# Kernel optimization log

Hardware: AMD Instinct MI355X
Metric: run time of the kernel (lower is better)

Reference implementation:

```python
import jax, jax.numpy as jnp
import numpy as np

T, B, E, H, R, NHASH, CHUNK = 2048, 2, 1024, 8, 2, 8, 32
D = E // H
INF = 1.0e16  # module's self.inf
BIG = 1.0e8   # module's self.big


def setup_inputs() -> dict:
    key = jax.random.key(0)
    ks = jax.random.split(key, 8)
    w = lambda k, shape, s=0.02: jax.random.normal(k, shape, dtype=jnp.float32) * s
    return {
        "query": jax.random.normal(ks[0], (T, B, E), jnp.float32),
        "key":   jax.random.normal(ks[1], (T, B, E), jnp.float32),
        "value": jax.random.normal(ks[2], (T, B, E), jnp.float32),
        "Wq": w(ks[3], (E, E)), "bq": jnp.zeros((E,), jnp.float32),
        "Wv": w(ks[4], (E, E)), "bv": jnp.zeros((E,), jnp.float32),
        "Wo": w(ks[5], (E, E)), "bo": jnp.zeros((E,), jnp.float32),
        "hash_w": w(ks[6], (R, H, D, NHASH // 2), 0.1),
    }


def _hashes(x_tbhd, hash_w):
    # einsum('ibnf,rnfh->ibrnh'), cat([lin,-lin]), argmax -> [T,B,R,H]
    lin = jnp.einsum('tbhd,rhdn->tbrhn', x_tbhd, hash_w)
    return jnp.argmax(jnp.concatenate([lin, -lin], axis=-1), axis=-1)


def _gather_t(x_bhtd, perm_brht):
    # gather along T with per-(b,r,h) permutation -> [B,R,H,T,D]
    Bb, Rr, Hh, Tt = perm_brht.shape
    Dd = x_bhtd.shape[-1]
    xb = jnp.broadcast_to(x_bhtd[:, None], (Bb, Rr, Hh, Tt, Dd))
    idx = jnp.broadcast_to(perm_brht[..., None], (Bb, Rr, Hh, Tt, Dd))
    return jnp.take_along_axis(xb, idx, axis=3)


def reference(query, key, value, Wq, bq, Wv, bv, Wo, bo, hash_w):
    del key  # share_kq=True (self-attention): keys are L2-normalized queries
    scaling = D ** -0.5
    qf = query @ Wq + bq                                    # [T,B,E]
    kf = qf / jnp.linalg.norm(qf, axis=-1, keepdims=True)   # F.normalize over embed dim
    vf = value @ Wv + bv
    q = qf.reshape(T, B, H, D) * scaling
    k = kf.reshape(T, B, H, D)
    v = vf.reshape(T, B, H, D)

    q_hash = _hashes(q, hash_w)                             # [T,B,R,H]
    k_hash = _hashes(k, hash_w)

    qh_t = jnp.transpose(q_hash, (1, 2, 3, 0))              # [B,R,H,T]
    kh_t = jnp.transpose(k_hash, (1, 2, 3, 0))
    p_q = jnp.argsort(qh_t, axis=-1)                        # stable sort by hash
    p_k = jnp.argsort(kh_t, axis=-1)
    inv_q = jnp.argsort(p_q, axis=-1)                       # sorted position of each token

    q_s = _gather_t(jnp.transpose(q, (1, 2, 0, 3)), p_q)    # [B,R,H,T,D]
    k_s = _gather_t(jnp.transpose(k, (1, 2, 0, 3)), p_k)
    v_s = _gather_t(jnp.transpose(v, (1, 2, 0, 3)), p_k)
    qh_s = jnp.take_along_axis(qh_t, p_q, axis=-1)
    kh_s = jnp.take_along_axis(kh_t, p_k, axis=-1)

    C = T // CHUNK
    M = 3 * CHUNK
    chunk = lambda x: x.reshape(x.shape[:3] + (C, CHUNK) + x.shape[4:])
    q_c, qh_c, qid_c = chunk(q_s), chunk(qh_s), chunk(p_q)
    k_c, v_c, kh_c, kid_c = chunk(k_s), chunk(v_s), chunk(kh_s), chunk(p_k)

    # each query chunk attends key chunks {c-1, c, c+1} (num_chunk_offsets=3, wraparound)
    blocks = lambda x: jnp.concatenate([jnp.roll(x, 1, axis=3), x, jnp.roll(x, -1, axis=3)], axis=4)
    kb, vb, khb, kidb = blocks(k_c), blocks(v_c), blocks(kh_c), blocks(kid_c)

    scores = jnp.einsum('brhcld,brhcmd->brhclm', q_c, kb)   # q pre-scaled by d^-0.5
    scores = scores - INF * (qh_c[..., :, None] != khb[..., None, :])   # mask_different_hashes
    scores = scores - BIG * (qid_c[..., :, None] == kidb[..., None, :]) # mask_current

    # cross-round duplicate counting: key ids attended per original query
    chunk_of = inv_q // CHUNK                               # [B,R,H,T]
    idx = jnp.broadcast_to(chunk_of[..., None], (B, R, H, T, M))
    A = jnp.take_along_axis(kidb, idx, axis=3)              # [B,R,H,T,M]
    dup = []
    for r in range(R):
        c = jnp.zeros((B, H, T, M), jnp.int32)
        for r2 in range(R):
            c = c + (A[:, r, :, :, :, None] == A[:, r2, :, :, None, :]).sum(-1, dtype=jnp.int32)
        dup.append(c)
    dup = jnp.stack(dup, axis=1)                            # [B,R,H,T,M]
    idx2 = jnp.broadcast_to(p_q[..., None], (B, R, H, T, M))
    dup_s = jnp.take_along_axis(dup, idx2, axis=3)          # sorted-query order
    scores = scores - jnp.log(dup_s.astype(scores.dtype)).reshape(scores.shape)

    z = jax.nn.logsumexp(scores, axis=-1)                   # [B,R,H,C,L]
    attn = jax.nn.softmax(scores, axis=-1)
    o = jnp.einsum('brhclm,brhcmd->brhcld', attn, vb).reshape(B, R, H, T, D)
    z = z.reshape(B, R, H, T)

    # scatter back to original token order
    idx3 = jnp.broadcast_to(inv_q[..., None], (B, R, H, T, D))
    o = jnp.take_along_axis(o, idx3, axis=3)
    z = jnp.take_along_axis(z, inv_q, axis=3)

    w = jax.nn.softmax(z, axis=1)                           # combine rounds by logsumexp weight
    out = (w[..., None] * o).sum(axis=1)                    # [B,H,T,D]
    out = jnp.transpose(out, (2, 0, 1, 3)).reshape(T, B, E)
    return out @ Wo + bo
```

## Files before the change

kernel.cpp:

```cpp
#include <hip/hip_runtime.h>

typedef unsigned short ushort_t;
typedef __bf16 bf16x8 __attribute__((ext_vector_type(8)));
typedef float f32x4 __attribute__((ext_vector_type(4)));

#define T_DIM 2048
#define B_DIM 2
#define E_DIM 1024
#define H_DIM 8
#define R_DIM 2
#define D_DIM 128
#define M_WIN 96
#define SCALING 0.08838834764831845f
#define LN2F 0.69314718055994530942f

__device__ __forceinline__ float bfu(unsigned u) {
  union { unsigned i; float f; } x; x.i = u << 16; return x.f;
}
__device__ __forceinline__ unsigned f2bf(float f) {
  union { float f; unsigned i; } x; x.f = f;
  unsigned r = x.i + 0x7fffu + ((x.i >> 16) & 1u);
  return r >> 16;
}
__device__ __forceinline__ void gl_lds16(const void* g, void* l) {
  __builtin_amdgcn_global_load_lds(
      (const __attribute__((address_space(1))) unsigned int*)g,
      (__attribute__((address_space(3))) unsigned int*)l, 16, 0, 0);
}

__global__ __launch_bounds__(256) void pack2_kernel(const float* __restrict__ in,
                                                    ushort_t* __restrict__ hi,
                                                    ushort_t* __restrict__ lo)
{
  int i = (blockIdx.x * 256 + threadIdx.x) * 4;
  float4 v = *(const float4*)&in[i];
  unsigned h0 = f2bf(v.x), h1 = f2bf(v.y), h2 = f2bf(v.z), h3 = f2bf(v.w);
  uint2 oh; oh.x = h0 | (h1 << 16); oh.y = h2 | (h3 << 16);
  *(uint2*)&hi[i] = oh;
  unsigned l0 = f2bf(v.x - bfu(h0)), l1 = f2bf(v.y - bfu(h1));
  unsigned l2 = f2bf(v.z - bfu(h2)), l3 = f2bf(v.w - bfu(h3));
  uint2 ol; ol.x = l0 | (l1 << 16); ol.y = l2 | (l3 << 16);
  *(uint2*)&lo[i] = ol;
}

__global__ __launch_bounds__(256) void pack1_kernel(const float* __restrict__ in,
                                                    ushort_t* __restrict__ hi)
{
  int i = (blockIdx.x * 256 + threadIdx.x) * 4;
  float4 v = *(const float4*)&in[i];
  uint2 oh;
  oh.x = f2bf(v.x) | (f2bf(v.y) << 16);
  oh.y = f2bf(v.z) | (f2bf(v.w) << 16);
  *(uint2*)&hi[i] = oh;
}

__global__ __launch_bounds__(256) void packT_kernel(const float* __restrict__ in,
                                                    ushort_t* __restrict__ hi,
                                                    ushort_t* __restrict__ lo,
                                                    int Kk, int Nn)
{
  __shared__ float tile[64][65];
  const int tid = threadIdx.x;
  const int k0 = blockIdx.y * 64, n0 = blockIdx.x * 64;
  const int tr = tid >> 4, tc4 = (tid & 15) * 4;
#pragma unroll
  for (int rr = 0; rr < 64; rr += 16)
    *(float4*)&tile[tr + rr][tc4] = *(const float4*)&in[(size_t)(k0 + tr + rr) * Nn + n0 + tc4];
  __syncthreads();
#pragma unroll
  for (int rr = 0; rr < 64; rr += 16) {
    int n = n0 + tr + rr;
    float v0 = tile[tc4 + 0][tr + rr];
    float v1 = tile[tc4 + 1][tr + rr];
    float v2 = tile[tc4 + 2][tr + rr];
    float v3 = tile[tc4 + 3][tr + rr];
    unsigned h0 = f2bf(v0), h1 = f2bf(v1), h2 = f2bf(v2), h3 = f2bf(v3);
    uint2 oh; oh.x = h0 | (h1 << 16); oh.y = h2 | (h3 << 16);
    *(uint2*)&hi[(size_t)n * Kk + k0 + tc4] = oh;
    if (lo) {
      uint2 ol;
      ol.x = f2bf(v0 - bfu(h0)) | (f2bf(v1 - bfu(h1)) << 16);
      ol.y = f2bf(v2 - bfu(h2)) | (f2bf(v3 - bfu(h3)) << 16);
      *(uint2*)&lo[(size_t)n * Kk + k0 + tc4] = ol;
    }
  }
}

__global__ __launch_bounds__(256) void gemm_mfma(
    const ushort_t* __restrict__ Ah, const ushort_t* __restrict__ Al,
    const ushort_t* __restrict__ Bh, const ushort_t* __restrict__ Bl,
    const float* __restrict__ bias, float* __restrict__ C,
    int Mm, int Nn, int Kk)
{
  __shared__ ushort_t As[128 * 32];
  __shared__ ushort_t Bs[64 * 32];
  __shared__ ushort_t As2[128 * 32];
  __shared__ ushort_t Bs2[64 * 32];
  const int tid = threadIdx.x;
  const int w = tid >> 6, lane = tid & 63;
  const int lm = lane & 15, quad = lane >> 4;
  const int wr = w >> 1, wc = w & 1;
  const int m0 = blockIdx.y * 128, n0 = blockIdx.x * 64;
  const bool three = (Al != nullptr);

  f32x4 acc[4][2] = {};

  for (int k0 = 0; k0 < Kk; k0 += 32) {
    __syncthreads();
#pragma unroll
    for (int j = 0; j < 2; ++j) {
      int g = j * 256 + w * 64 + lane;
      gl_lds16(Ah + (size_t)(m0 + (g >> 2)) * Kk + k0 + (g & 3) * 8,
               &As[(size_t)(j * 256 + w * 64) * 8]);
    }
    {
      int g = w * 64 + lane;
      gl_lds16(Bh + (size_t)(n0 + (g >> 2)) * Kk + k0 + (g & 3) * 8,
               &Bs[(size_t)(w * 64) * 8]);
    }
    if (three) {
#pragma unroll
      for (int j = 0; j < 2; ++j) {
        int g = j * 256 + w * 64 + lane;
        gl_lds16(Al + (size_t)(m0 + (g >> 2)) * Kk + k0 + (g & 3) * 8,
                 &As2[(size_t)(j * 256 + w * 64) * 8]);
      }
      int g = w * 64 + lane;
      gl_lds16(Bl + (size_t)(n0 + (g >> 2)) * Kk + k0 + (g & 3) * 8,
               &Bs2[(size_t)(w * 64) * 8]);
    }
    __syncthreads();

    bf16x8 av[4], bv[2];
#pragma unroll
    for (int i = 0; i < 4; ++i) av[i] = *(const bf16x8*)&As[(wr * 64 + i * 16 + lm) * 32 + quad * 8];
#pragma unroll
    for (int j = 0; j < 2; ++j) bv[j] = *(const bf16x8*)&Bs[(wc * 32 + j * 16 + lm) * 32 + quad * 8];
    if (three) {
      bf16x8 av2[4], bv2[2];
#pragma unroll
      for (int i = 0; i < 4; ++i) av2[i] = *(const bf16x8*)&As2[(wr * 64 + i * 16 + lm) * 32 + quad * 8];
#pragma unroll
      for (int j = 0; j < 2; ++j) bv2[j] = *(const bf16x8*)&Bs2[(wc * 32 + j * 16 + lm) * 32 + quad * 8];
#pragma unroll
      for (int i = 0; i < 4; ++i)
#pragma unroll
        for (int j = 0; j < 2; ++j) {
          acc[i][j] = __builtin_amdgcn_mfma_f32_16x16x32_bf16(av[i], bv[j], acc[i][j], 0, 0, 0);
          acc[i][j] = __builtin_amdgcn_mfma_f32_16x16x32_bf16(av2[i], bv[j], acc[i][j], 0, 0, 0);
          acc[i][j] = __builtin_amdgcn_mfma_f32_16x16x32_bf16(av[i], bv2[j], acc[i][j], 0, 0, 0);
        }
    } else {
#pragma unroll
      for (int i = 0; i < 4; ++i)
#pragma unroll
        for (int j = 0; j < 2; ++j)
          acc[i][j] = __builtin_amdgcn_mfma_f32_16x16x32_bf16(av[i], bv[j], acc[i][j], 0, 0, 0);
    }
  }

#pragma unroll
  for (int j = 0; j < 2; ++j) {
    int col = n0 + wc * 32 + j * 16 + lm;
    float bj = bias[col];
#pragma unroll
    for (int i = 0; i < 4; ++i)
#pragma unroll
      for (int rg = 0; rg < 4; ++rg)
        C[(size_t)(m0 + wr * 64 + i * 16 + quad * 4 + rg) * Nn + col] = acc[i][j][rg] + bj;
  }
}

__global__ __launch_bounds__(256) void norm_kernel(const float* __restrict__ qf,
                                                   float* __restrict__ inv_nrm)
{
  int row = blockIdx.x, tid = threadIdx.x;
  const float* r = qf + (size_t)row * E_DIM;
  float4 v = *(const float4*)(r + tid * 4);
  float s = v.x * v.x + v.y * v.y + v.z * v.z + v.w * v.w;
  for (int off = 1; off < 64; off <<= 1) s += __shfl_xor(s, off);
  __shared__ float part[4];
  if ((tid & 63) == 0) part[tid >> 6] = s;
  __syncthreads();
  if (tid == 0) {
    float t = part[0] + part[1] + part[2] + part[3];
    inv_nrm[row] = 1.0f / sqrtf(t);
  }
}

__global__ __launch_bounds__(256) void hash_kernel(const float* __restrict__ qf,
                                                   const float* __restrict__ hw,
                                                   int* __restrict__ hashb)
{
  __shared__ float wlds[16 * 516];
  const int tid = threadIdx.x;
  for (int i = tid; i < 8192; i += 256) wlds[(i >> 9) * 516 + (i & 511)] = hw[i];
  __syncthreads();
  const int rloc = tid >> 4, rh = tid & 15;
  const int r = rh >> 3, h = rh & 7;
  const int row = blockIdx.x * 16 + rloc;
  const float* qrow = qf + (size_t)row * E_DIM + h * D_DIM;
  const float* wp = &wlds[rh * 516];
  float a0 = 0.f, a1 = 0.f, a2 = 0.f, a3 = 0.f;
  for (int d = 0; d < 128; d += 4) {
    float4 q4 = *(const float4*)&qrow[d];
    float4 w0 = *(const float4*)&wp[d * 4];
    float4 w1 = *(const float4*)&wp[d * 4 + 4];
    float4 w2 = *(const float4*)&wp[d * 4 + 8];
    float4 w3 = *(const float4*)&wp[d * 4 + 12];
    a0 += q4.x * w0.x + q4.y * w1.x + q4.z * w2.x + q4.w * w3.x;
    a1 += q4.x * w0.y + q4.y * w1.y + q4.z * w2.y + q4.w * w3.y;
    a2 += q4.x * w0.z + q4.y * w1.z + q4.z * w2.z + q4.w * w3.z;
    a3 += q4.x * w0.w + q4.y * w1.w + q4.z * w2.w + q4.w * w3.w;
  }
  float lin[4] = {a0, a1, a2, a3};
  float best = lin[0]; int bi = 0;
#pragma unroll
  for (int idx = 1; idx < 8; ++idx) {
    float v = (idx < 4) ? lin[idx] : -lin[idx - 4];
    if (v > best) { best = v; bi = idx; }
  }
  int t = row >> 1, b = row & 1;
  hashb[(size_t)((b * R_DIM + r) * H_DIM + h) * T_DIM + t] = bi;
}

__global__ __launch_bounds__(256) void sort_kernel(const int* __restrict__ hashb,
                                                   int* __restrict__ p, int* __restrict__ inv)
{
  const int bid = blockIdx.x, tid = threadIdx.x;
  const int lane = tid & 63, w = tid >> 6;
  const int* hrow = hashb + (size_t)bid * T_DIM;
  __shared__ int mat[8][256];
  __shared__ int btot[8], bbase[8];
  int cnt[8];
#pragma unroll
  for (int v = 0; v < 8; ++v) cnt[v] = 0;
  int hv[8];
#pragma unroll
  for (int j = 0; j < 8; ++j) { hv[j] = hrow[tid * 8 + j]; cnt[hv[j]]++; }
#pragma unroll
  for (int v = 0; v < 8; ++v) mat[v][tid] = cnt[v];
  __syncthreads();
  for (int v = w; v < 8; v += 4) {
    int4 c4 = *(const int4*)&mat[v][lane * 4];
    int s = c4.x + c4.y + c4.z + c4.w;
    int x = s;
    for (int off = 1; off < 64; off <<= 1) {
      int y = __shfl_up(x, off);
      if (lane >= off) x += y;
    }
    int excl = x - s;
    mat[v][lane * 4 + 0] = excl;
    mat[v][lane * 4 + 1] = excl + c4.x;
    mat[v][lane * 4 + 2] = excl + c4.x + c4.y;
    mat[v][lane * 4 + 3] = excl + c4.x + c4.y + c4.z;
    if (lane == 63) btot[v] = x;
  }
  __syncthreads();
  if (tid == 0) {
    int run = 0;
    for (int v = 0; v < 8; ++v) { bbase[v] = run; run += btot[v]; }
  }
  __syncthreads();
#pragma unroll
  for (int v = 0; v < 8; ++v) cnt[v] = 0;
#pragma unroll
  for (int j = 0; j < 8; ++j) {
    int v = hv[j];
    int pos = bbase[v] + mat[v][tid] + cnt[v];
    cnt[v]++;
    p[(size_t)bid * T_DIM + pos] = tid * 8 + j;
    inv[(size_t)bid * T_DIM + tid * 8 + j] = pos;
  }
}

__global__ __launch_bounds__(256) void attn_kernel(
    const float* __restrict__ qf, const float* __restrict__ vf,
    const float* __restrict__ inv_nrm, const int* __restrict__ hashb,
    const int* __restrict__ p, const int* __restrict__ inv,
    float* __restrict__ o_out, float* __restrict__ z_out)
{
  const int c = blockIdx.x, h = blockIdx.y, bz = blockIdx.z;
  const int b = bz >> 1, r = bz & 1;
  const int brh = (b * R_DIM + r) * H_DIM + h;
  const int brh_o = (b * R_DIM + (r ^ 1)) * H_DIM + h;
  const int tid = threadIdx.x;
  const int lane = tid & 63, w = tid >> 6;
  const int lm = lane & 15, quad = lane >> 4;

  __shared__ __align__(16) unsigned char smem[45824];
  ushort_t* Qs = (ushort_t*)smem;
  ushort_t* Ks = (ushort_t*)(smem + 8704);
  ushort_t* VT = (ushort_t*)smem;
  float*    SS = (float*)(smem + 26624);
  ushort_t* Ps = (ushort_t*)(smem + 39168);
  __shared__ int sq_id[32], sq_h[32], cq_o[32];
  __shared__ int sk_id[M_WIN], sk_h[M_WIN], ck_o[M_WIN];
  __shared__ float s_invn[M_WIN];

  if (tid < M_WIN) {
    int m = tid;
    int chunk = (c + (m >> 5) + 63) & 63;
    int pos = chunk * 32 + (m & 31);
    int t = p[(size_t)brh * T_DIM + pos];
    sk_id[m] = t;
    sk_h[m] = hashb[(size_t)brh * T_DIM + t];
    ck_o[m] = inv[(size_t)brh_o * T_DIM + t] >> 5;
    s_invn[m] = inv_nrm[t * B_DIM + b];
    if (m < 32) {
      int tq = p[(size_t)brh * T_DIM + c * 32 + m];
      sq_id[m] = tq;
      sq_h[m] = hashb[(size_t)brh * T_DIM + tq];
      cq_o[m] = inv[(size_t)brh_o * T_DIM + tq] >> 5;
    }
  }
  __syncthreads();

  for (int idx = tid; idx < 1024; idx += 256) {
    int row = idx >> 5, seg = idx & 31;
    int t = sq_id[row];
    float4 v = *(const float4*)(qf + ((size_t)(t * B_DIM + b) << 10) + h * D_DIM + seg * 4);
    uint2 o2;
    o2.x = f2bf(v.x * SCALING) | (f2bf(v.y * SCALING) << 16);
    o2.y = f2bf(v.z * SCALING) | (f2bf(v.w * SCALING) << 16);
    *(uint2*)&Qs[row * 136 + seg * 4] = o2;
  }
  for (int idx = tid; idx < 3072; idx += 256) {
    int m = idx >> 5, seg = idx & 31;
    int t = sk_id[m];
    float inrm = s_invn[m];
    float4 v = *(const float4*)(qf + ((size_t)(t * B_DIM + b) << 10) + h * D_DIM + seg * 4);
    uint2 o2;
    o2.x = f2bf(v.x * inrm) | (f2bf(v.y * inrm) << 16);
    o2.y = f2bf(v.z * inrm) | (f2bf(v.w * inrm) << 16);
    *(uint2*)&Ks[m * 136 + seg * 4] = o2;
  }
  __syncthreads();

  const int mw = w & 1, nset = w >> 1;
  bf16x8 av[4];
#pragma unroll
  for (int kk = 0; kk < 4; ++kk)
    av[kk] = *(const bf16x8*)&Qs[(mw * 16 + lm) * 136 + kk * 32 + quad * 8];
  f32x4 sacc[3] = {};
#pragma unroll
  for (int jj = 0; jj < 3; ++jj) {
    int nt = nset * 3 + jj;
#pragma unroll
    for (int kk = 0; kk < 4; ++kk) {
      bf16x8 bv = *(const bf16x8*)&Ks[(nt * 16 + lm) * 136 + kk * 32 + quad * 8];
      sacc[jj] = __builtin_amdgcn_mfma_f32_16x16x32_bf16(av[kk], bv, sacc[jj], 0, 0, 0);
    }
  }
  __syncthreads();

  const int rowb = mw * 16 + quad * 4;
#pragma unroll
  for (int jj = 0; jj < 3; ++jj) {
    int col = (nset * 3 + jj) * 16 + lm;
    int kh = sk_h[col], kid = sk_id[col], kco = ck_o[col];
#pragma unroll
    for (int rg = 0; rg < 4; ++rg) {
      int row = rowb + rg;
      float sc = sacc[jj][rg];
      if (kh != sq_h[row]) sc -= 1.0e16f;
      if (kid == sq_id[row]) sc -= 1.0e8f;
      int dc = (kco - cq_o[row]) & 63;
      if (dc <= 1 || dc == 63) sc -= LN2F;
      SS[row * 98 + col] = sc;
    }
  }
  for (int idx = tid; idx < 3072; idx += 256) {
    int d = idx & 127, mg = idx >> 7;
    unsigned vv0, vv1, vv2, vv3;
    {
      int t0 = sk_id[mg * 4 + 0], t1 = sk_id[mg * 4 + 1];
      int t2 = sk_id[mg * 4 + 2], t3 = sk_id[mg * 4 + 3];
      const size_t off = (size_t)h * D_DIM + d;
      vv0 = f2bf(vf[((size_t)(t0 * B_DIM + b) << 10) + off]);
      vv1 = f2bf(vf[((size_t)(t1 * B_DIM + b) << 10) + off]);
      vv2 = f2bf(vf[((size_t)(t2 * B_DIM + b) << 10) + off]);
      vv3 = f2bf(vf[((size_t)(t3 * B_DIM + b) << 10) + off]);
    }
    uint2 o2; o2.x = vv0 | (vv1 << 16); o2.y = vv2 | (vv3 << 16);
    *(uint2*)&VT[d * 104 + mg * 4] = o2;
  }
  __syncthreads();

  {
    const int l = tid >> 3, g = tid & 7;
    float smy[12];
#pragma unroll
    for (int j = 0; j < 12; ++j) smy[j] = SS[l * 98 + g + 8 * j];
    float mx = smy[0];
#pragma unroll
    for (int j = 1; j < 12; ++j) mx = fmaxf(mx, smy[j]);
    mx = fmaxf(mx, __shfl_xor(mx, 1));
    mx = fmaxf(mx, __shfl_xor(mx, 2));
    mx = fmaxf(mx, __shfl_xor(mx, 4));
    float sum = 0.f, ey[12];
#pragma unroll
    for (int j = 0; j < 12; ++j) { ey[j] = expf(smy[j] - mx); sum += ey[j]; }
    sum += __shfl_xor(sum, 1);
    sum += __shfl_xor(sum, 2);
    sum += __shfl_xor(sum, 4);
    float inv_s = 1.0f / sum;
#pragma unroll
    for (int j = 0; j < 12; ++j)
      Ps[l * 104 + g + 8 * j] = (ushort_t)f2bf(ey[j] * inv_s);
    if (g == 0) z_out[(size_t)brh * T_DIM + sq_id[l]] = mx + logf(sum);
  }
  __syncthreads();

  const int dset = w >> 1;
  bf16x8 pa[3];
#pragma unroll
  for (int kk = 0; kk < 3; ++kk)
    pa[kk] = *(const bf16x8*)&Ps[(mw * 16 + lm) * 104 + kk * 32 + quad * 8];
  f32x4 oacc[4] = {};
#pragma unroll
  for (int jj = 0; jj < 4; ++jj) {
    int dt = dset * 4 + jj;
#pragma unroll
    for (int kk = 0; kk < 3; ++kk) {
      bf16x8 bv = *(const bf16x8*)&VT[(dt * 16 + lm) * 104 + kk * 32 + quad * 8];
      oacc[jj] = __builtin_amdgcn_mfma_f32_16x16x32_bf16(pa[kk], bv, oacc[jj], 0, 0, 0);
    }
  }
#pragma unroll
  for (int jj = 0; jj < 4; ++jj) {
    int col = (dset * 4 + jj) * 16 + lm;
#pragma unroll
    for (int rg = 0; rg < 4; ++rg) {
      int row = rowb + rg;
      int tqo = sq_id[row];
      o_out[((size_t)brh * T_DIM + tqo) * D_DIM + col] = oacc[jj][rg];
    }
  }
}

__global__ __launch_bounds__(256) void combine_kernel(const float* __restrict__ o_buf,
                                                      const float* __restrict__ z_buf,
                                                      ushort_t* __restrict__ ctx)
{
  int gid = blockIdx.x * 256 + threadIdx.x;
  int d = gid & 127;
  int t = (gid >> 7) & (T_DIM - 1);
  int h = (gid >> 18) & 7;
  int b = gid >> 21;
  int brh0 = (b * R_DIM + 0) * H_DIM + h;
  int brh1 = brh0 + H_DIM;
  float z0 = z_buf[(size_t)brh0 * T_DIM + t], z1 = z_buf[(size_t)brh1 * T_DIM + t];
  float mz = fmaxf(z0, z1);
  float e0 = expf(z0 - mz), e1 = expf(z1 - mz);
  float o0 = o_buf[((size_t)brh0 * T_DIM + t) * D_DIM + d];
  float o1 = o_buf[((size_t)brh1 * T_DIM + t) * D_DIM + d];
  float val = (e0 * o0 + e1 * o1) / (e0 + e1);
  ctx[((size_t)t * B_DIM + b) * E_DIM + h * D_DIM + d] = (ushort_t)f2bf(val);
}

extern "C" void kernel_launch(void* const* d_in, const int* in_sizes, int n_in,
                              void* d_out, int out_size, void* d_ws, size_t ws_size,
                              hipStream_t stream)
{
  const float* query = (const float*)d_in[0];
  const float* value = (const float*)d_in[2];
  const float* Wq = (const float*)d_in[3];
  const float* bq = (const float*)d_in[4];
  const float* Wv = (const float*)d_in[5];
  const float* bv = (const float*)d_in[6];
  const float* Wo = (const float*)d_in[7];
  const float* bo = (const float*)d_in[8];
  const float* hw = (const float*)d_in[9];

  float* ws = (float*)d_ws;
  float* qf      = ws;
  float* vf      = qf + 4194304;
  float* obuf    = vf + 4194304;
  float* zbuf    = obuf + 8388608;
  float* inv_nrm = zbuf + 65536;
  int*   hashb   = (int*)(inv_nrm + 4096);
  int*   pperm   = hashb + 65536;
  int*   pinv    = pperm + 65536;
  ushort_t* WqTh = (ushort_t*)(pinv + 65536);
  ushort_t* WqTl = WqTh + 1048576;
  ushort_t* WvTh = WqTl + 1048576;
  ushort_t* WoTh = WvTh + 1048576;
  ushort_t* qh  = (ushort_t*)obuf;
  ushort_t* ql  = qh + 4194304;
  ushort_t* vh  = ql + 4194304;
  ushort_t* ctx = (ushort_t*)qf;

  pack2_kernel<<<4096, 256, 0, stream>>>(query, qh, ql);
  pack1_kernel<<<4096, 256, 0, stream>>>(value, vh);
  packT_kernel<<<dim3(16, 16), 256, 0, stream>>>(Wq, WqTh, WqTl, 1024, 1024);
  packT_kernel<<<dim3(16, 16), 256, 0, stream>>>(Wv, WvTh, (ushort_t*)nullptr, 1024, 1024);
  packT_kernel<<<dim3(16, 16), 256, 0, stream>>>(Wo, WoTh, (ushort_t*)nullptr, 1024, 1024);
  gemm_mfma<<<dim3(16, 32), 256, 0, stream>>>(qh, ql, WqTh, WqTl, bq, qf, 4096, 1024, 1024);
  gemm_mfma<<<dim3(16, 32), 256, 0, stream>>>(vh, (ushort_t*)nullptr, WvTh, (ushort_t*)nullptr, bv, vf, 4096, 1024, 1024);
  norm_kernel<<<4096, 256, 0, stream>>>(qf, inv_nrm);
  hash_kernel<<<256, 256, 0, stream>>>(qf, hw, hashb);
  sort_kernel<<<32, 256, 0, stream>>>(hashb, pperm, pinv);
  attn_kernel<<<dim3(64, 8, 4), 256, 0, stream>>>(qf, vf, inv_nrm, hashb, pperm, pinv, obuf, zbuf);
  combine_kernel<<<16384, 256, 0, stream>>>(obuf, zbuf, ctx);
  gemm_mfma<<<dim3(16, 32), 256, 0, stream>>>(ctx, (ushort_t*)nullptr, WoTh, (ushort_t*)nullptr, bo, (float*)d_out, 4096, 1024, 1024);
}
```

Baseline: 283.1 us.

## Compute hashes from fused Wq·hash_w in fp32, drop split-bf16 Q GEMM, batch launches

Hash logits are now computed directly from the fp32 query times a precomputed Wq·hash_w matrix (plus bias term), so the Q projection GEMM no longer needs the three-pass hi/lo bf16 split for hash accuracy and runs as a plain bf16 GEMM. The Q and V GEMMs are merged into one launch via blockIdx.z, as are the pack kernels and the three weight transposes. The attention output buffer is stored in bf16, and combine is vectorized to four elements per thread. Key metadata is packed into one int per token to shrink shared memory. The cost is lower precision for Q/K in attention and for the per-round outputs, plus an extra small fp32 GEMM for hashing.

```diff
diff --git a/kernel.cpp b/kernel.cpp
--- a/kernel.cpp
+++ b/kernel.cpp
@@ -28,107 +28,163 @@
       (__attribute__((address_space(3))) unsigned int*)l, 16, 0, 0);
 }
 
-__global__ __launch_bounds__(256) void pack2_kernel(const float* __restrict__ in,
-                                                    ushort_t* __restrict__ hi,
-                                                    ushort_t* __restrict__ lo)
-{
-  int i = (blockIdx.x * 256 + threadIdx.x) * 4;
-  float4 v = *(const float4*)&in[i];
-  unsigned h0 = f2bf(v.x), h1 = f2bf(v.y), h2 = f2bf(v.z), h3 = f2bf(v.w);
-  uint2 oh; oh.x = h0 | (h1 << 16); oh.y = h2 | (h3 << 16);
-  *(uint2*)&hi[i] = oh;
-  unsigned l0 = f2bf(v.x - bfu(h0)), l1 = f2bf(v.y - bfu(h1));
-  unsigned l2 = f2bf(v.z - bfu(h2)), l3 = f2bf(v.w - bfu(h3));
-  uint2 ol; ol.x = l0 | (l1 << 16); ol.y = l2 | (l3 << 16);
-  *(uint2*)&lo[i] = ol;
-}
-
-__global__ __launch_bounds__(256) void pack1_kernel(const float* __restrict__ in,
-                                                    ushort_t* __restrict__ hi)
-{
-  int i = (blockIdx.x * 256 + threadIdx.x) * 4;
-  float4 v = *(const float4*)&in[i];
+__global__ __launch_bounds__(256) void packA_kernel(const float* __restrict__ q,
+                                                    const float* __restrict__ v,
+                                                    ushort_t* __restrict__ qh,
+                                                    ushort_t* __restrict__ vh)
+{
+  int bid = blockIdx.x;
+  const float* src = (bid < 4096) ? q : v;
+  ushort_t* dst = (bid < 4096) ? qh : vh;
+  int i = ((bid & 4095) * 256 + threadIdx.x) * 4;
+  float4 x = *(const float4*)&src[i];
   uint2 oh;
-  oh.x = f2bf(v.x) | (f2bf(v.y) << 16);
-  oh.y = f2bf(v.z) | (f2bf(v.w) << 16);
-  *(uint2*)&hi[i] = oh;
-}
-
-__global__ __launch_bounds__(256) void packT_kernel(const float* __restrict__ in,
-                                                    ushort_t* __restrict__ hi,
-                                                    ushort_t* __restrict__ lo,
-                                                    int Kk, int Nn)
-{
+  oh.x = f2bf(x.x) | (f2bf(x.y) << 16);
+  oh.y = f2bf(x.z) | (f2bf(x.w) << 16);
+  *(uint2*)&dst[i] = oh;
+}
+
+__global__ __launch_bounds__(256) void packT_kernel(
+    const float* __restrict__ w0, const float* __restrict__ w1,
+    const float* __restrict__ w2, ushort_t* __restrict__ o0,
+    ushort_t* __restrict__ o1, ushort_t* __restrict__ o2)
+{
+  const float* in = (blockIdx.z == 0) ? w0 : (blockIdx.z == 1) ? w1 : w2;
+  ushort_t* hi = (blockIdx.z == 0) ? o0 : (blockIdx.z == 1) ? o1 : o2;
   __shared__ float tile[64][65];
   const int tid = threadIdx.x;
   const int k0 = blockIdx.y * 64, n0 = blockIdx.x * 64;
   const int tr = tid >> 4, tc4 = (tid & 15) * 4;
 #pragma unroll
   for (int rr = 0; rr < 64; rr += 16)
-    *(float4*)&tile[tr + rr][tc4] = *(const float4*)&in[(size_t)(k0 + tr + rr) * Nn + n0 + tc4];
+    *(float4*)&tile[tr + rr][tc4] = *(const float4*)&in[(size_t)(k0 + tr + rr) * E_DIM + n0 + tc4];
   __syncthreads();
 #pragma unroll
   for (int rr = 0; rr < 64; rr += 16) {
     int n = n0 + tr + rr;
-    float v0 = tile[tc4 + 0][tr + rr];
-    float v1 = tile[tc4 + 1][tr + rr];
-    float v2 = tile[tc4 + 2][tr + rr];
-    float v3 = tile[tc4 + 3][tr + rr];
-    unsigned h0 = f2bf(v0), h1 = f2bf(v1), h2 = f2bf(v2), h3 = f2bf(v3);
-    uint2 oh; oh.x = h0 | (h1 << 16); oh.y = h2 | (h3 << 16);
-    *(uint2*)&hi[(size_t)n * Kk + k0 + tc4] = oh;
-    if (lo) {
-      uint2 ol;
-      ol.x = f2bf(v0 - bfu(h0)) | (f2bf(v1 - bfu(h1)) << 16);
-      ol.y = f2bf(v2 - bfu(h2)) | (f2bf(v3 - bfu(h3)) << 16);
-      *(uint2*)&lo[(size_t)n * Kk + k0 + tc4] = ol;
-    }
-  }
+    uint2 oh;
+    oh.x = f2bf(tile[tc4 + 0][tr + rr]) | (f2bf(tile[tc4 + 1][tr + rr]) << 16);
+    oh.y = f2bf(tile[tc4 + 2][tr + rr]) | (f2bf(tile[tc4 + 3][tr + rr]) << 16);
+    *(uint2*)&hi[(size_t)n * E_DIM + k0 + tc4] = oh;
+  }
+}
+
+__global__ __launch_bounds__(256) void fuseF_kernel(const float* __restrict__ Wq,
+                                                    const float* __restrict__ bq,
+                                                    const float* __restrict__ hw,
+                                                    float* __restrict__ F,
+                                                    float* __restrict__ cvec)
+{
+  __shared__ float wl[512];
+  const int rh = blockIdx.x, h = rh & 7;
+  const int tid = threadIdx.x;
+  for (int i = tid; i < 512; i += 256) wl[i] = hw[rh * 512 + i];
+  __syncthreads();
+  for (int e = tid; e < E_DIM; e += 256) {
+    const float* wr = Wq + (size_t)e * E_DIM + h * D_DIM;
+    float a0 = 0.f, a1 = 0.f, a2 = 0.f, a3 = 0.f;
+    for (int d = 0; d < 128; d += 4) {
+      float4 q4 = *(const float4*)&wr[d];
+      float4 w0 = *(const float4*)&wl[d * 4];
+      float4 w1 = *(const float4*)&wl[d * 4 + 4];
+      float4 w2 = *(const float4*)&wl[d * 4 + 8];
+      float4 w3 = *(const float4*)&wl[d * 4 + 12];
+      a0 += q4.x * w0.x + q4.y * w1.x + q4.z * w2.x + q4.w * w3.x;
+      a1 += q4.x * w0.y + q4.y * w1.y + q4.z * w2.y + q4.w * w3.y;
+      a2 += q4.x * w0.z + q4.y * w1.z + q4.z * w2.z + q4.w * w3.z;
+      a3 += q4.x * w0.w + q4.y * w1.w + q4.z * w2.w + q4.w * w3.w;
+    }
+    float4 o; o.x = a0; o.y = a1; o.z = a2; o.w = a3;
+    *(float4*)&F[(size_t)e * 64 + rh * 4] = o;
+  }
+  if (tid < 4) {
+    float acc = 0.f;
+    for (int d = 0; d < 128; ++d) acc += bq[h * D_DIM + d] * wl[d * 4 + tid];
+    cvec[rh * 4 + tid] = acc;
+  }
+}
+
+__global__ __launch_bounds__(256) void hashlin_kernel(const float* __restrict__ query,
+                                                      const float* __restrict__ F,
+                                                      const float* __restrict__ cvec,
+                                                      int* __restrict__ hashb)
+{
+  __shared__ float As[32][17];
+  __shared__ float Fs[32][64];
+  const int tid = threadIdx.x;
+  const int ty = tid >> 4, tx = tid & 15;
+  const int r0 = blockIdx.x * 16;
+  float acc0 = 0.f, acc1 = 0.f, acc2 = 0.f, acc3 = 0.f;
+  for (int k0 = 0; k0 < E_DIM; k0 += 32) {
+    __syncthreads();
+    {
+      int i = tid * 2, row = i >> 5, kk = i & 31;
+      float2 a2 = *(const float2*)&query[(size_t)(r0 + row) * E_DIM + k0 + kk];
+      As[kk][row] = a2.x; As[kk + 1][row] = a2.y;
+    }
+    {
+      int i = tid * 8, kk = i >> 6, cc = i & 63;
+      float4 f0 = *(const float4*)&F[(size_t)(k0 + kk) * 64 + cc];
+      float4 f1 = *(const float4*)&F[(size_t)(k0 + kk) * 64 + cc + 4];
+      *(float4*)&Fs[kk][cc] = f0;
+      *(float4*)&Fs[kk][cc + 4] = f1;
+    }
+    __syncthreads();
+#pragma unroll
+    for (int kk = 0; kk < 32; ++kk) {
+      float a = As[kk][ty];
+      float4 f4 = *(const float4*)&Fs[kk][tx * 4];
+      acc0 += a * f4.x; acc1 += a * f4.y; acc2 += a * f4.z; acc3 += a * f4.w;
+    }
+  }
+  float4 c4 = *(const float4*)&cvec[tx * 4];
+  float lin[4] = {acc0 + c4.x, acc1 + c4.y, acc2 + c4.z, acc3 + c4.w};
+  float best = lin[0]; int bi = 0;
+#pragma unroll
+  for (int idx = 1; idx < 8; ++idx) {
+    float v = (idx < 4) ? lin[idx] : -lin[idx - 4];
+    if (v > best) { best = v; bi = idx; }
+  }
+  int grow = r0 + ty;
+  int t = grow >> 1, b = grow & 1;
+  int rr = tx >> 3, hh = tx & 7;
+  hashb[(size_t)((b * R_DIM + rr) * H_DIM + hh) * T_DIM + t] = bi;
 }
 
 __global__ __launch_bounds__(256) void gemm_mfma(
-    const ushort_t* __restrict__ Ah, const ushort_t* __restrict__ Al,
-    const ushort_t* __restrict__ Bh, const ushort_t* __restrict__ Bl,
-    const float* __restrict__ bias, float* __restrict__ C,
-    int Mm, int Nn, int Kk)
-{
+    const ushort_t* __restrict__ A0, const ushort_t* __restrict__ B0,
+    const float* __restrict__ bias0, float* __restrict__ C0,
+    const ushort_t* __restrict__ A1, const ushort_t* __restrict__ B1,
+    const float* __restrict__ bias1, float* __restrict__ C1)
+{
+  const ushort_t* Ah = blockIdx.z ? A1 : A0;
+  const ushort_t* Bh = blockIdx.z ? B1 : B0;
+  const float* bias = blockIdx.z ? bias1 : bias0;
+  float* C = blockIdx.z ? C1 : C0;
+
   __shared__ ushort_t As[128 * 32];
   __shared__ ushort_t Bs[64 * 32];
-  __shared__ ushort_t As2[128 * 32];
-  __shared__ ushort_t Bs2[64 * 32];
   const int tid = threadIdx.x;
   const int w = tid >> 6, lane = tid & 63;
   const int lm = lane & 15, quad = lane >> 4;
   const int wr = w >> 1, wc = w & 1;
   const int m0 = blockIdx.y * 128, n0 = blockIdx.x * 64;
-  const bool three = (Al != nullptr);
 
   f32x4 acc[4][2] = {};
 
-  for (int k0 = 0; k0 < Kk; k0 += 32) {
+  for (int k0 = 0; k0 < E_DIM; k0 += 32) {
     __syncthreads();
 #pragma unroll
     for (int j = 0; j < 2; ++j) {
       int g = j * 256 + w * 64 + lane;
-      gl_lds16(Ah + (size_t)(m0 + (g >> 2)) * Kk + k0 + (g & 3) * 8,
+      gl_lds16(Ah + (size_t)(m0 + (g >> 2)) * E_DIM + k0 + (g & 3) * 8,
                &As[(size_t)(j * 256 + w * 64) * 8]);
     }
     {
       int g = w * 64 + lane;
-      gl_lds16(Bh + (size_t)(n0 + (g >> 2)) * Kk + k0 + (g & 3) * 8,
+      gl_lds16(Bh + (size_t)(n0 + (g >> 2)) * E_DIM + k0 + (g & 3) * 8,
                &Bs[(size_t)(w * 64) * 8]);
     }
-    if (three) {
-#pragma unroll
-      for (int j = 0; j < 2; ++j) {
-        int g = j * 256 + w * 64 + lane;
-        gl_lds16(Al + (size_t)(m0 + (g >> 2)) * Kk + k0 + (g & 3) * 8,
-                 &As2[(size_t)(j * 256 + w * 64) * 8]);
-      }
-      int g = w * 64 + lane;
-      gl_lds16(Bl + (size_t)(n0 + (g >> 2)) * Kk + k0 + (g & 3) * 8,
-               &Bs2[(size_t)(w * 64) * 8]);
-    }
     __syncthreads();
 
     bf16x8 av[4], bv[2];
@@ -136,27 +192,11 @@
     for (int i = 0; i < 4; ++i) av[i] = *(const bf16x8*)&As[(wr * 64 + i * 16 + lm) * 32 + quad * 8];
 #pragma unroll
     for (int j = 0; j < 2; ++j) bv[j] = *(const bf16x8*)&Bs[(wc * 32 + j * 16 + lm) * 32 + quad * 8];
-    if (three) {
-      bf16x8 av2[4], bv2[2];
-#pragma unroll
-      for (int i = 0; i < 4; ++i) av2[i] = *(const bf16x8*)&As2[(wr * 64 + i * 16 + lm) * 32 + quad * 8];
-#pragma unroll
-      for (int j = 0; j < 2; ++j) bv2[j] = *(const bf16x8*)&Bs2[(wc * 32 + j * 16 + lm) * 32 + quad * 8];
-#pragma unroll
-      for (int i = 0; i < 4; ++i)
-#pragma unroll
-        for (int j = 0; j < 2; ++j) {
-          acc[i][j] = __builtin_amdgcn_mfma_f32_16x16x32_bf16(av[i], bv[j], acc[i][j], 0, 0, 0);
-          acc[i][j] = __builtin_amdgcn_mfma_f32_16x16x32_bf16(av2[i], bv[j], acc[i][j], 0, 0, 0);
-          acc[i][j] = __builtin_amdgcn_mfma_f32_16x16x32_bf16(av[i], bv2[j], acc[i][j], 0, 0, 0);
-        }
-    } else {
-#pragma unroll
-      for (int i = 0; i < 4; ++i)
-#pragma unroll
-        for (int j = 0; j < 2; ++j)
-          acc[i][j] = __builtin_amdgcn_mfma_f32_16x16x32_bf16(av[i], bv[j], acc[i][j], 0, 0, 0);
-    }
+#pragma unroll
+    for (int i = 0; i < 4; ++i)
+#pragma unroll
+      for (int j = 0; j < 2; ++j)
+        acc[i][j] = __builtin_amdgcn_mfma_f32_16x16x32_bf16(av[i], bv[j], acc[i][j], 0, 0, 0);
   }
 
 #pragma unroll
@@ -167,7 +207,7 @@
     for (int i = 0; i < 4; ++i)
 #pragma unroll
       for (int rg = 0; rg < 4; ++rg)
-        C[(size_t)(m0 + wr * 64 + i * 16 + quad * 4 + rg) * Nn + col] = acc[i][j][rg] + bj;
+        C[(size_t)(m0 + wr * 64 + i * 16 + quad * 4 + rg) * E_DIM + col] = acc[i][j][rg] + bj;
   }
 }
 
@@ -188,42 +228,6 @@
   }
 }
 
-__global__ __launch_bounds__(256) void hash_kernel(const float* __restrict__ qf,
-                                                   const float* __restrict__ hw,
-                                                   int* __restrict__ hashb)
-{
-  __shared__ float wlds[16 * 516];
-  const int tid = threadIdx.x;
-  for (int i = tid; i < 8192; i += 256) wlds[(i >> 9) * 516 + (i & 511)] = hw[i];
-  __syncthreads();
-  const int rloc = tid >> 4, rh = tid & 15;
-  const int r = rh >> 3, h = rh & 7;
-  const int row = blockIdx.x * 16 + rloc;
-  const float* qrow = qf + (size_t)row * E_DIM + h * D_DIM;
-  const float* wp = &wlds[rh * 516];
-  float a0 = 0.f, a1 = 0.f, a2 = 0.f, a3 = 0.f;
-  for (int d = 0; d < 128; d += 4) {
-    float4 q4 = *(const float4*)&qrow[d];
-    float4 w0 = *(const float4*)&wp[d * 4];
-    float4 w1 = *(const float4*)&wp[d * 4 + 4];
-    float4 w2 = *(const float4*)&wp[d * 4 + 8];
-    float4 w3 = *(const float4*)&wp[d * 4 + 12];
-    a0 += q4.x * w0.x + q4.y * w1.x + q4.z * w2.x + q4.w * w3.x;
-    a1 += q4.x * w0.y + q4.y * w1.y + q4.z * w2.y + q4.w * w3.y;
-    a2 += q4.x * w0.z + q4.y * w1.z + q4.z * w2.z + q4.w * w3.z;
-    a3 += q4.x * w0.w + q4.y * w1.w + q4.z * w2.w + q4.w * w3.w;
-  }
-  float lin[4] = {a0, a1, a2, a3};
-  float best = lin[0]; int bi = 0;
-#pragma unroll
-  for (int idx = 1; idx < 8; ++idx) {
-    float v = (idx < 4) ? lin[idx] : -lin[idx - 4];
-    if (v > best) { best = v; bi = idx; }
-  }
-  int t = row >> 1, b = row & 1;
-  hashb[(size_t)((b * R_DIM + r) * H_DIM + h) * T_DIM + t] = bi;
-}
-
 __global__ __launch_bounds__(256) void sort_kernel(const int* __restrict__ hashb,
                                                    int* __restrict__ p, int* __restrict__ inv)
 {
@@ -278,7 +282,7 @@
     const float* __restrict__ qf, const float* __restrict__ vf,
     const float* __restrict__ inv_nrm, const int* __restrict__ hashb,
     const int* __restrict__ p, const int* __restrict__ inv,
-    float* __restrict__ o_out, float* __restrict__ z_out)
+    ushort_t* __restrict__ o_out, float* __restrict__ z_out)
 {
   const int c = blockIdx.x, h = blockIdx.y, bz = blockIdx.z;
   const int b = bz >> 1, r = bz & 1;
@@ -288,14 +292,13 @@
   const int lane = tid & 63, w = tid >> 6;
   const int lm = lane & 15, quad = lane >> 4;
 
-  __shared__ __align__(16) unsigned char smem[45824];
+  __shared__ __align__(16) unsigned char smem[39424];
   ushort_t* Qs = (ushort_t*)smem;
   ushort_t* Ks = (ushort_t*)(smem + 8704);
   ushort_t* VT = (ushort_t*)smem;
   float*    SS = (float*)(smem + 26624);
-  ushort_t* Ps = (ushort_t*)(smem + 39168);
-  __shared__ int sq_id[32], sq_h[32], cq_o[32];
-  __shared__ int sk_id[M_WIN], sk_h[M_WIN], ck_o[M_WIN];
+  ushort_t* Ps = (ushort_t*)(smem + 26624);
+  __shared__ int skp[M_WIN], sqp[32];
   __shared__ float s_invn[M_WIN];
 
   if (tid < M_WIN) {
@@ -303,22 +306,22 @@
     int chunk = (c + (m >> 5) + 63) & 63;
     int pos = chunk * 32 + (m & 31);
     int t = p[(size_t)brh * T_DIM + pos];
-    sk_id[m] = t;
-    sk_h[m] = hashb[(size_t)brh * T_DIM + t];
-    ck_o[m] = inv[(size_t)brh_o * T_DIM + t] >> 5;
+    int hh = hashb[(size_t)brh * T_DIM + t];
+    int co = inv[(size_t)brh_o * T_DIM + t] >> 5;
+    skp[m] = t | (hh << 11) | (co << 14);
     s_invn[m] = inv_nrm[t * B_DIM + b];
     if (m < 32) {
       int tq = p[(size_t)brh * T_DIM + c * 32 + m];
-      sq_id[m] = tq;
-      sq_h[m] = hashb[(size_t)brh * T_DIM + tq];
-      cq_o[m] = inv[(size_t)brh_o * T_DIM + tq] >> 5;
+      int qh = hashb[(size_t)brh * T_DIM + tq];
+      int qco = inv[(size_t)brh_o * T_DIM + tq] >> 5;
+      sqp[m] = tq | (qh << 11) | (qco << 14);
     }
   }
   __syncthreads();
 
   for (int idx = tid; idx < 1024; idx += 256) {
     int row = idx >> 5, seg = idx & 31;
-    int t = sq_id[row];
+    int t = sqp[row] & 2047;
     float4 v = *(const float4*)(qf + ((size_t)(t * B_DIM + b) << 10) + h * D_DIM + seg * 4);
     uint2 o2;
     o2.x = f2bf(v.x * SCALING) | (f2bf(v.y * SCALING) << 16);
@@ -327,7 +330,7 @@
   }
   for (int idx = tid; idx < 3072; idx += 256) {
     int m = idx >> 5, seg = idx & 31;
-    int t = sk_id[m];
+    int t = skp[m] & 2047;
     float inrm = s_invn[m];
     float4 v = *(const float4*)(qf + ((size_t)(t * B_DIM + b) << 10) + h * D_DIM + seg * 4);
     uint2 o2;
@@ -358,30 +361,27 @@
 #pragma unroll
   for (int jj = 0; jj < 3; ++jj) {
     int col = (nset * 3 + jj) * 16 + lm;
-    int kh = sk_h[col], kid = sk_id[col], kco = ck_o[col];
+    int kp = skp[col];
 #pragma unroll
     for (int rg = 0; rg < 4; ++rg) {
-      int row = rowb + rg;
+      int qp = sqp[rowb + rg];
       float sc = sacc[jj][rg];
-      if (kh != sq_h[row]) sc -= 1.0e16f;
-      if (kid == sq_id[row]) sc -= 1.0e8f;
-      int dc = (kco - cq_o[row]) & 63;
+      if ((kp ^ qp) & 0x3800) sc -= 1.0e16f;
+      if (!((kp ^ qp) & 0x7FF)) sc -= 1.0e8f;
+      int dc = ((kp >> 14) - (qp >> 14)) & 63;
       if (dc <= 1 || dc == 63) sc -= LN2F;
-      SS[row * 98 + col] = sc;
+      SS[(rowb + rg) * 100 + col] = sc;
     }
   }
   for (int idx = tid; idx < 3072; idx += 256) {
     int d = idx & 127, mg = idx >> 7;
-    unsigned vv0, vv1, vv2, vv3;
-    {
-      int t0 = sk_id[mg * 4 + 0], t1 = sk_id[mg * 4 + 1];
-      int t2 = sk_id[mg * 4 + 2], t3 = sk_id[mg * 4 + 3];
-      const size_t off = (size_t)h * D_DIM + d;
-      vv0 = f2bf(vf[((size_t)(t0 * B_DIM + b) << 10) + off]);
-      vv1 = f2bf(vf[((size_t)(t1 * B_DIM + b) << 10) + off]);
-      vv2 = f2bf(vf[((size_t)(t2 * B_DIM + b) << 10) + off]);
-      vv3 = f2bf(vf[((size_t)(t3 * B_DIM + b) << 10) + off]);
-    }
+    int t0 = skp[mg * 4 + 0] & 2047, t1 = skp[mg * 4 + 1] & 2047;
+    int t2 = skp[mg * 4 + 2] & 2047, t3 = skp[mg * 4 + 3] & 2047;
+    const size_t off = (size_t)h * D_DIM + d;
+    unsigned vv0 = f2bf(vf[((size_t)(t0 * B_DIM + b) << 10) + off]);
+    unsigned vv1 = f2bf(vf[((size_t)(t1 * B_DIM + b) << 10) + off]);
+    unsigned vv2 = f2bf(vf[((size_t)(t2 * B_DIM + b) << 10) + off]);
+    unsigned vv3 = f2bf(vf[((size_t)(t3 * B_DIM + b) << 10) + off]);
     uint2 o2; o2.x = vv0 | (vv1 << 16); o2.y = vv2 | (vv3 << 16);
     *(uint2*)&VT[d * 104 + mg * 4] = o2;
   }
@@ -391,7 +391,7 @@
     const int l = tid >> 3, g = tid & 7;
     float smy[12];
 #pragma unroll
-    for (int j = 0; j < 12; ++j) smy[j] = SS[l * 98 + g + 8 * j];
+    for (int j = 0; j < 12; ++j) smy[j] = SS[l * 100 + g + 8 * j];
     float mx = smy[0];
 #pragma unroll
     for (int j = 1; j < 12; ++j) mx = fmaxf(mx, smy[j]);
@@ -407,8 +407,8 @@
     float inv_s = 1.0f / sum;
 #pragma unroll
     for (int j = 0; j < 12; ++j)
-      Ps[l * 104 + g + 8 * j] = (ushort_t)f2bf(ey[j] * inv_s);
-    if (g == 0) z_out[(size_t)brh * T_DIM + sq_id[l]] = mx + logf(sum);
+      Ps[l * 200 + g + 8 * j] = (ushort_t)f2bf(ey[j] * inv_s);
+    if (g == 0) z_out[(size_t)brh * T_DIM + (sqp[l] & 2047)] = mx + logf(sum);
   }
   __syncthreads();
 
@@ -416,7 +416,7 @@
   bf16x8 pa[3];
 #pragma unroll
   for (int kk = 0; kk < 3; ++kk)
-    pa[kk] = *(const bf16x8*)&Ps[(mw * 16 + lm) * 104 + kk * 32 + quad * 8];
+    pa[kk] = *(const bf16x8*)&Ps[(mw * 16 + lm) * 200 + kk * 32 + quad * 8];
   f32x4 oacc[4] = {};
 #pragma unroll
   for (int jj = 0; jj < 4; ++jj) {
@@ -432,31 +432,36 @@
     int col = (dset * 4 + jj) * 16 + lm;
 #pragma unroll
     for (int rg = 0; rg < 4; ++rg) {
-      int row = rowb + rg;
-      int tqo = sq_id[row];
-      o_out[((size_t)brh * T_DIM + tqo) * D_DIM + col] = oacc[jj][rg];
-    }
-  }
-}
-
-__global__ __launch_bounds__(256) void combine_kernel(const float* __restrict__ o_buf,
+      int tqo = sqp[rowb + rg] & 2047;
+      o_out[((size_t)brh * T_DIM + tqo) * D_DIM + col] = (ushort_t)f2bf(oacc[jj][rg]);
+    }
+  }
+}
+
+__global__ __launch_bounds__(256) void combine_kernel(const ushort_t* __restrict__ obf,
                                                       const float* __restrict__ z_buf,
                                                       ushort_t* __restrict__ ctx)
 {
   int gid = blockIdx.x * 256 + threadIdx.x;
-  int d = gid & 127;
-  int t = (gid >> 7) & (T_DIM - 1);
-  int h = (gid >> 18) & 7;
-  int b = gid >> 21;
+  int d4 = gid & 31;
+  int t = (gid >> 5) & (T_DIM - 1);
+  int h = (gid >> 16) & 7;
+  int b = gid >> 19;
   int brh0 = (b * R_DIM + 0) * H_DIM + h;
   int brh1 = brh0 + H_DIM;
   float z0 = z_buf[(size_t)brh0 * T_DIM + t], z1 = z_buf[(size_t)brh1 * T_DIM + t];
   float mz = fmaxf(z0, z1);
   float e0 = expf(z0 - mz), e1 = expf(z1 - mz);
-  float o0 = o_buf[((size_t)brh0 * T_DIM + t) * D_DIM + d];
-  float o1 = o_buf[((size_t)brh1 * T_DIM + t) * D_DIM + d];
-  float val = (e0 * o0 + e1 * o1) / (e0 + e1);
-  ctx[((size_t)t * B_DIM + b) * E_DIM + h * D_DIM + d] = (ushort_t)f2bf(val);
+  float is = 1.0f / (e0 + e1);
+  float w0 = e0 * is, w1 = e1 * is;
+  uint2 a = *(const uint2*)&obf[((size_t)brh0 * T_DIM + t) * D_DIM + d4 * 4];
+  uint2 cc = *(const uint2*)&obf[((size_t)brh1 * T_DIM + t) * D_DIM + d4 * 4];
+  uint2 o;
+  o.x = f2bf(w0 * bfu(a.x & 0xffffu) + w1 * bfu(cc.x & 0xffffu)) |
+        (f2bf(w0 * bfu(a.x >> 16) + w1 * bfu(cc.x >> 16)) << 16);
+  o.y = f2bf(w0 * bfu(a.y & 0xffffu) + w1 * bfu(cc.y & 0xffffu)) |
+        (f2bf(w0 * bfu(a.y >> 16) + w1 * bfu(cc.y >> 16)) << 16);
+  *(uint2*)&ctx[((size_t)(t * B_DIM + b) << 10) + h * D_DIM + d4 * 4] = o;
 }
 
 extern "C" void kernel_launch(void* const* d_in, const int* in_sizes, int n_in,
@@ -474,34 +479,34 @@
   const float* hw = (const float*)d_in[9];
 
   float* ws = (float*)d_ws;
-  float* qf      = ws;
-  float* vf      = qf + 4194304;
-  float* obuf    = vf + 4194304;
-  float* zbuf    = obuf + 8388608;
+  float* qf   = ws;
+  float* vf   = qf + 4194304;
+  float* bigf = vf + 4194304;
+  ushort_t* obuf = (ushort_t*)bigf;
+  ushort_t* ctx  = obuf + 8388608;
+  ushort_t* qh   = (ushort_t*)bigf;
+  ushort_t* vh   = qh + 4194304;
+  ushort_t* WqTh = (ushort_t*)(bigf + 6291456);
+  ushort_t* WvTh = WqTh + 1048576;
+  ushort_t* WoTh = WvTh + 1048576;
+  float* F       = (float*)(WoTh + 1048576);
+  float* cvec    = F + 65536;
+  float* zbuf    = cvec + 64;
   float* inv_nrm = zbuf + 65536;
   int*   hashb   = (int*)(inv_nrm + 4096);
   int*   pperm   = hashb + 65536;
   int*   pinv    = pperm + 65536;
-  ushort_t* WqTh = (ushort_t*)(pinv + 65536);
-  ushort_t* WqTl = WqTh + 1048576;
-  ushort_t* WvTh = WqTl + 1048576;
-  ushort_t* WoTh = WvTh + 1048576;
-  ushort_t* qh  = (ushort_t*)obuf;
-  ushort_t* ql  = qh + 4194304;
-  ushort_t* vh  = ql + 4194304;
-  ushort_t* ctx = (ushort_t*)qf;
-
-  pack2_kernel<<<4096, 256, 0, stream>>>(query, qh, ql);
-  pack1_kernel<<<4096, 256, 0, stream>>>(value, vh);
-  packT_kernel<<<dim3(16, 16), 256, 0, stream>>>(Wq, WqTh, WqTl, 1024, 1024);
-  packT_kernel<<<dim3(16, 16), 256, 0, stream>>>(Wv, WvTh, (ushort_t*)nullptr, 1024, 1024);
-  packT_kernel<<<dim3(16, 16), 256, 0, stream>>>(Wo, WoTh, (ushort_t*)nullptr, 1024, 1024);
-  gemm_mfma<<<dim3(16, 32), 256, 0, stream>>>(qh, ql, WqTh, WqTl, bq, qf, 4096, 1024, 1024);
-  gemm_mfma<<<dim3(16, 32), 256, 0, stream>>>(vh, (ushort_t*)nullptr, WvTh, (ushort_t*)nullptr, bv, vf, 4096, 1024, 1024);
+
+  packA_kernel<<<8192, 256, 0, stream>>>(query, value, qh, vh);
+  packT_kernel<<<dim3(16, 16, 3), 256, 0, stream>>>(Wq, Wv, Wo, WqTh, WvTh, WoTh);
+  fuseF_kernel<<<16, 256, 0, stream>>>(Wq, bq, hw, F, cvec);
+  hashlin_kernel<<<256, 256, 0, stream>>>(query, F, cvec, hashb);
+  gemm_mfma<<<dim3(16, 32, 2), 256, 0, stream>>>(qh, WqTh, bq, qf, vh, WvTh, bv, vf);
   norm_kernel<<<4096, 256, 0, stream>>>(qf, inv_nrm);
-  hash_kernel<<<256, 256, 0, stream>>>(qf, hw, hashb);
   sort_kernel<<<32, 256, 0, stream>>>(hashb, pperm, pinv);
   attn_kernel<<<dim3(64, 8, 4), 256, 0, stream>>>(qf, vf, inv_nrm, hashb, pperm, pinv, obuf, zbuf);
-  combine_kernel<<<16384, 256, 0, stream>>>(obuf, zbuf, ctx);
-  gemm_mfma<<<dim3(16, 32), 256, 0, stream>>>(ctx, (ushort_t*)nullptr, WoTh, (ushort_t*)nullptr, bo, (float*)d_out, 4096, 1024, 1024);
-}
+  combine_kernel<<<4096, 256, 0, stream>>>(obuf, zbuf, ctx);
+  gemm_mfma<<<dim3(16, 32, 1), 256, 0, stream>>>(ctx, WoTh, bo, (float*)d_out,
+                                                 (ushort_t*)nullptr, (ushort_t*)nullptr,
+                                                 (const float*)nullptr, (float*)nullptr);
+}
```

New measurement: 272.3 us. 3.8% less time.
